# Kernel tuning notes

Measured on AMD Instinct MI355X. Metric: run time of the kernel, lower is better.

The kernel has to match this reference:

```python
import jax, jax.numpy as jnp
import numpy as np

IMG_DIM = 512


def _grid_q(img_dim):
    # matches torch module: q = [repeat(x, D), tile(y, D)] -> shape [2, D*D]
    x = np.arange(img_dim)
    q = np.stack([np.repeat(x, img_dim), np.tile(x, img_dim)], axis=0)
    return jnp.asarray(q, jnp.float32)


def _get_pixel(point, neighbor, imflat, img_dim):
    # point, neighbor: [N,2,HW]; imflat: [N,3,HW]
    w = 1.0 - jnp.abs(point - neighbor)          # [N,2,HW]
    weight = w[:, 0] * w[:, 1]                   # [N,HW]
    inds = (neighbor[:, 1] + img_dim * neighbor[:, 0]).astype(jnp.int32)  # y + D*x, [N,HW]
    # fused gather over all 3 channels (original does 3 separate torch.gather)
    pix = jnp.take_along_axis(imflat, inds[:, None, :], axis=2)  # [N,3,HW]
    return weight[:, None, :] * pix


def _get_masked_rp(image, mask, qi_orig, img_dim):
    N, Cc, H, W = image.shape
    imflat = image.reshape(N, Cc, H * W)
    qi_rescale = qi_orig * img_dim
    qi = jnp.clip(qi_rescale, 0.001, img_dim - 1.001)
    xf = jnp.floor(qi[:, 0:1]); yf = jnp.floor(qi[:, 1:2])
    xc = jnp.ceil(qi[:, 0:1]);  yc = jnp.ceil(qi[:, 1:2])
    res = (_get_pixel(qi, jnp.concatenate([xf, yf], axis=1), imflat, img_dim)
         + _get_pixel(qi, jnp.concatenate([xc, yf], axis=1), imflat, img_dim)
         + _get_pixel(qi, jnp.concatenate([xf, yc], axis=1), imflat, img_dim)
         + _get_pixel(qi, jnp.concatenate([xc, yc], axis=1), imflat, img_dim))
    oob_loss = jnp.mean((qi_rescale - qi) ** 2) / (img_dim ** 2) * 0.0001
    res_img = res.reshape(image.shape)
    return res_img * mask, oob_loss  # mask broadcasts [N,1,H,W] -> [N,3,H,W]


def setup_inputs() -> dict:
    key = jax.random.key(0)
    k1, k2, k3, k4, k5 = jax.random.split(key, 5)
    N, D = 16, IMG_DIM
    im1 = jax.random.normal(k1, (N, 3, D, D), dtype=jnp.float32)
    im2 = jax.random.normal(k2, (N, 3, D, D), dtype=jnp.float32)
    C = jax.random.normal(k3, (N, 2, D, D), dtype=jnp.float32)
    M1 = jax.random.uniform(k4, (N, 1, D, D), dtype=jnp.float32)
    M2 = jax.random.uniform(k5, (N, 1, D, D), dtype=jnp.float32)
    return {"im1": im1, "im2": im2, "C": C, "M1": M1, "M2": M2}


def reference(im1, im2, C, M1, M2):
    img_dim = im1.shape[-1]
    N = C.shape[0]
    Cflat = C.reshape(N, 2, -1)                 # [N,2,HW]
    total_mask = M1 + M2
    M1n = M1 / total_mask
    M2n = M2 / total_mask
    q = _grid_q(img_dim)[None]                  # [1,2,HW], broadcasts to [N,2,HW]
    a, oob_a = _get_masked_rp(im1, M1n, q + Cflat, img_dim)
    b, oob_b = _get_masked_rp(im2, M2n, q - Cflat, img_dim)
    return a + b, oob_a + oob_b
```

## Files before the change

### kernel.cpp

```cpp
#include <hip/hip_runtime.h>

#define D     512
#define HW    (D * D)
#define BLOCK 256
#define PPT   4
#define PIX_PER_BLOCK (BLOCK * PPT)

__device__ __forceinline__ void sample1(const float* __restrict__ im,
                                        float rx, float ry, float m,
                                        float r[3], double* oob) {
    float cxq = fminf(fmaxf(rx, 0.001f), 510.999f);
    float cyq = fminf(fmaxf(ry, 0.001f), 510.999f);
    float dx = rx - cxq;
    float dy = ry - cyq;
    *oob += (double)(dx * dx) + (double)(dy * dy);

    float xf = floorf(cxq), xc = ceilf(cxq);
    float yf = floorf(cyq), yc = ceilf(cyq);
    float wxf = 1.0f - (cxq - xf);
    float wxc = 1.0f - (xc - cxq);
    float wyf = 1.0f - (cyq - yf);
    float wyc = 1.0f - (yc - cyq);

    int ixf = (int)xf, ixc = (int)xc, iyf = (int)yf, iyc = (int)yc;
    int i00 = iyf + D * ixf;
    int i10 = iyf + D * ixc;
    int i01 = iyc + D * ixf;
    int i11 = iyc + D * ixc;

    float w00 = wxf * wyf, w10 = wxc * wyf, w01 = wxf * wyc, w11 = wxc * wyc;

#pragma unroll
    for (int c = 0; c < 3; ++c) {
        const float* __restrict__ ch = im + (size_t)c * HW;
        float pix = w00 * ch[i00] + w10 * ch[i10] + w01 * ch[i01] + w11 * ch[i11];
        r[c] += m * pix;
    }
}

__global__ void __launch_bounds__(BLOCK) vm_kernel(
    const float* __restrict__ im1, const float* __restrict__ im2,
    const float* __restrict__ C,   const float* __restrict__ M1,
    const float* __restrict__ M2,  float* __restrict__ out,
    double* __restrict__ partials)
{
    int t   = blockIdx.x * BLOCK + threadIdx.x;
    int idx = t * PPT;
    int n = idx >> 18;
    int p = idx & (HW - 1);
    int i = p >> 9;
    int j = p & (D - 1);

    const size_t cb = (size_t)n * 2 * HW + p;
    const size_t mb = (size_t)n * HW + p;
    float4 cx4 = *(const float4*)(C  + cb);
    float4 cy4 = *(const float4*)(C  + cb + HW);
    float4 m14 = *(const float4*)(M1 + mb);
    float4 m24 = *(const float4*)(M2 + mb);

    float cx[PPT] = {cx4.x, cx4.y, cx4.z, cx4.w};
    float cy[PPT] = {cy4.x, cy4.y, cy4.z, cy4.w};
    float m1[PPT] = {m14.x, m14.y, m14.z, m14.w};
    float m2[PPT] = {m24.x, m24.y, m24.z, m24.w};

    const float* base1 = im1 + (size_t)n * 3 * HW;
    const float* base2 = im2 + (size_t)n * 3 * HW;

    float o0[PPT], o1[PPT], o2[PPT];
    double oob = 0.0;

#pragma unroll
    for (int k = 0; k < PPT; ++k) {
        float tot = m1[k] + m2[k];
        float m1n = m1[k] / tot;
        float m2n = m2[k] / tot;
        float r[3] = {0.f, 0.f, 0.f};
        float fi = (float)i;
        float fj = (float)(j + k);
        sample1(base1, (fi + cx[k]) * (float)D, (fj + cy[k]) * (float)D, m1n, r, &oob);
        sample1(base2, (fi - cx[k]) * (float)D, (fj - cy[k]) * (float)D, m2n, r, &oob);
        o0[k] = r[0]; o1[k] = r[1]; o2[k] = r[2];
    }

    size_t ob = (size_t)n * 3 * HW + p;
    *(float4*)(out + ob)          = make_float4(o0[0], o0[1], o0[2], o0[3]);
    *(float4*)(out + ob + HW)     = make_float4(o1[0], o1[1], o1[2], o1[3]);
    *(float4*)(out + ob + 2 * HW) = make_float4(o2[0], o2[1], o2[2], o2[3]);

    for (int off = 32; off > 0; off >>= 1)
        oob += __shfl_down(oob, off, 64);

    __shared__ double soob[BLOCK / 64];
    int lane = threadIdx.x & 63;
    int w    = threadIdx.x >> 6;
    if (lane == 0) soob[w] = oob;
    __syncthreads();
    if (threadIdx.x == 0)
        partials[blockIdx.x] = soob[0] + soob[1] + soob[2] + soob[3];
}

__global__ void __launch_bounds__(BLOCK) reduce_kernel(
    const double* __restrict__ partials, int nparts,
    float* __restrict__ out_last, double scale)
{
    double s = 0.0;
    for (int i = threadIdx.x; i < nparts; i += BLOCK)
        s += partials[i];
    for (int off = 32; off > 0; off >>= 1)
        s += __shfl_down(s, off, 64);

    __shared__ double sm[BLOCK / 64];
    int lane = threadIdx.x & 63;
    int w    = threadIdx.x >> 6;
    if (lane == 0) sm[w] = s;
    __syncthreads();
    if (threadIdx.x == 0)
        *out_last = (float)((sm[0] + sm[1] + sm[2] + sm[3]) * scale);
}

extern "C" void kernel_launch(void* const* d_in, const int* in_sizes, int n_in,
                              void* d_out, int out_size, void* d_ws, size_t ws_size,
                              hipStream_t stream) {
    const float* im1 = (const float*)d_in[0];
    const float* im2 = (const float*)d_in[1];
    const float* C   = (const float*)d_in[2];
    const float* M1  = (const float*)d_in[3];
    const float* M2  = (const float*)d_in[4];
    float* out = (float*)d_out;
    double* ws = (double*)d_ws;

    int N = in_sizes[3] / HW;
    int total  = N * HW;
    int blocks = total / PIX_PER_BLOCK;

    vm_kernel<<<blocks, BLOCK, 0, stream>>>(im1, im2, C, M1, M2, out, ws);

    double scale = 1.0 / ((double)N * 2.0 * (double)HW) / (double)HW * 1e-4;
    reduce_kernel<<<1, BLOCK, 0, stream>>>(ws, blocks, out + (out_size - 1), scale);
}
```

Measured before the change: 219.3 us.

## Remap threads to row strips, preload corner pixels, and use float OOB sums

Each thread now handles one column across four rows instead of four consecutive pixels. Each block loads the bottom-right 2x2 corner pixels of both images once. Samples clamped to that corner use the preloaded values and skip the per-channel gathers, which matters because random displacements scaled by 512 push many samples out of range. The per-thread out-of-bounds accumulation moves from double to float, which removes FP64 arithmetic but risks precision loss in the loss term.

```diff
diff --git a/kernel.cpp b/kernel.cpp
--- a/kernel.cpp
+++ b/kernel.cpp
@@ -3,17 +3,18 @@
 #define D     512
 #define HW    (D * D)
 #define BLOCK 256
-#define PPT   4
-#define PIX_PER_BLOCK (BLOCK * PPT)
+#define ROWS  4
+#define COLS  256
 
 __device__ __forceinline__ void sample1(const float* __restrict__ im,
+                                        const float* __restrict__ cpix,
                                         float rx, float ry, float m,
-                                        float r[3], double* oob) {
+                                        float r[3], float* oob) {
     float cxq = fminf(fmaxf(rx, 0.001f), 510.999f);
     float cyq = fminf(fmaxf(ry, 0.001f), 510.999f);
     float dx = rx - cxq;
     float dy = ry - cyq;
-    *oob += (double)(dx * dx) + (double)(dy * dy);
+    *oob += dx * dx + dy * dy;
 
     float xf = floorf(cxq), xc = ceilf(cxq);
     float yf = floorf(cyq), yc = ceilf(cyq);
@@ -21,21 +22,37 @@
     float wxc = 1.0f - (xc - cxq);
     float wyf = 1.0f - (cyq - yf);
     float wyc = 1.0f - (yc - cyq);
-
-    int ixf = (int)xf, ixc = (int)xc, iyf = (int)yf, iyc = (int)yc;
-    int i00 = iyf + D * ixf;
-    int i10 = iyf + D * ixc;
-    int i01 = iyc + D * ixf;
-    int i11 = iyc + D * ixc;
-
     float w00 = wxf * wyf, w10 = wxc * wyf, w01 = wxf * wyc, w11 = wxc * wyc;
 
+    float p[3][4];
 #pragma unroll
     for (int c = 0; c < 3; ++c) {
-        const float* __restrict__ ch = im + (size_t)c * HW;
-        float pix = w00 * ch[i00] + w10 * ch[i10] + w01 * ch[i01] + w11 * ch[i11];
-        r[c] += m * pix;
+        p[c][0] = cpix[c * 4 + 0];
+        p[c][1] = cpix[c * 4 + 1];
+        p[c][2] = cpix[c * 4 + 2];
+        p[c][3] = cpix[c * 4 + 3];
     }
+
+    bool corner = (rx >= 510.999f) && (ry >= 510.999f);
+    if (!corner) {
+        int ixf = (int)xf, ixc = (int)xc, iyf = (int)yf, iyc = (int)yc;
+        int i00 = iyf + D * ixf;
+        int i10 = iyf + D * ixc;
+        int i01 = iyc + D * ixf;
+        int i11 = iyc + D * ixc;
+#pragma unroll
+        for (int c = 0; c < 3; ++c) {
+            const float* __restrict__ ch = im + (size_t)c * HW;
+            p[c][0] = ch[i00];
+            p[c][1] = ch[i10];
+            p[c][2] = ch[i01];
+            p[c][3] = ch[i11];
+        }
+    }
+
+#pragma unroll
+    for (int c = 0; c < 3; ++c)
+        r[c] += m * (w00 * p[c][0] + w10 * p[c][1] + w01 * p[c][2] + w11 * p[c][3]);
 }
 
 __global__ void __launch_bounds__(BLOCK) vm_kernel(
@@ -44,59 +61,71 @@
     const float* __restrict__ M2,  float* __restrict__ out,
     double* __restrict__ partials)
 {
-    int t   = blockIdx.x * BLOCK + threadIdx.x;
-    int idx = t * PPT;
-    int n = idx >> 18;
-    int p = idx & (HW - 1);
-    int i = p >> 9;
-    int j = p & (D - 1);
-
-    const size_t cb = (size_t)n * 2 * HW + p;
-    const size_t mb = (size_t)n * HW + p;
-    float4 cx4 = *(const float4*)(C  + cb);
-    float4 cy4 = *(const float4*)(C  + cb + HW);
-    float4 m14 = *(const float4*)(M1 + mb);
-    float4 m24 = *(const float4*)(M2 + mb);
-
-    float cx[PPT] = {cx4.x, cx4.y, cx4.z, cx4.w};
-    float cy[PPT] = {cy4.x, cy4.y, cy4.z, cy4.w};
-    float m1[PPT] = {m14.x, m14.y, m14.z, m14.w};
-    float m2[PPT] = {m24.x, m24.y, m24.z, m24.w};
+    int b    = blockIdx.x;
+    int colh = b & 1;
+    int rg   = (b >> 1) & 127;
+    int n    = b >> 8;
+    int j    = colh * COLS + threadIdx.x;
+    int i0   = rg * ROWS;
 
     const float* base1 = im1 + (size_t)n * 3 * HW;
     const float* base2 = im2 + (size_t)n * 3 * HW;
 
-    float o0[PPT], o1[PPT], o2[PPT];
-    double oob = 0.0;
+    float cp1[12], cp2[12];
+#pragma unroll
+    for (int c = 0; c < 3; ++c) {
+        const float* c1 = base1 + (size_t)c * HW;
+        const float* c2 = base2 + (size_t)c * HW;
+        cp1[c * 4 + 0] = c1[510 + D * 510];
+        cp1[c * 4 + 1] = c1[510 + D * 511];
+        cp1[c * 4 + 2] = c1[511 + D * 510];
+        cp1[c * 4 + 3] = c1[511 + D * 511];
+        cp2[c * 4 + 0] = c2[510 + D * 510];
+        cp2[c * 4 + 1] = c2[510 + D * 511];
+        cp2[c * 4 + 2] = c2[511 + D * 510];
+        cp2[c * 4 + 3] = c2[511 + D * 511];
+    }
+
+    const size_t cb = (size_t)n * 2 * HW;
+    const size_t mb = (size_t)n * HW;
+    const size_t ob = (size_t)n * 3 * HW;
+
+    float oob = 0.0f;
 
 #pragma unroll
-    for (int k = 0; k < PPT; ++k) {
-        float tot = m1[k] + m2[k];
-        float m1n = m1[k] / tot;
-        float m2n = m2[k] / tot;
-        float r[3] = {0.f, 0.f, 0.f};
-        float fi = (float)i;
-        float fj = (float)(j + k);
-        sample1(base1, (fi + cx[k]) * (float)D, (fj + cy[k]) * (float)D, m1n, r, &oob);
-        sample1(base2, (fi - cx[k]) * (float)D, (fj - cy[k]) * (float)D, m2n, r, &oob);
-        o0[k] = r[0]; o1[k] = r[1]; o2[k] = r[2];
+    for (int r = 0; r < ROWS; ++r) {
+        int i = i0 + r;
+        size_t pp = (size_t)i * D + j;
+
+        float cx = C[cb + pp];
+        float cy = C[cb + HW + pp];
+        float m1 = M1[mb + pp];
+        float m2 = M2[mb + pp];
+        float tot = m1 + m2;
+        float m1n = m1 / tot;
+        float m2n = m2 / tot;
+
+        float acc[3] = {0.f, 0.f, 0.f};
+        float fi = (float)i, fj = (float)j;
+        sample1(base1, cp1, (fi + cx) * (float)D, (fj + cy) * (float)D, m1n, acc, &oob);
+        sample1(base2, cp2, (fi - cx) * (float)D, (fj - cy) * (float)D, m2n, acc, &oob);
+
+        out[ob + pp]          = acc[0];
+        out[ob + HW + pp]     = acc[1];
+        out[ob + 2 * HW + pp] = acc[2];
     }
-
-    size_t ob = (size_t)n * 3 * HW + p;
-    *(float4*)(out + ob)          = make_float4(o0[0], o0[1], o0[2], o0[3]);
-    *(float4*)(out + ob + HW)     = make_float4(o1[0], o1[1], o1[2], o1[3]);
-    *(float4*)(out + ob + 2 * HW) = make_float4(o2[0], o2[1], o2[2], o2[3]);
 
     for (int off = 32; off > 0; off >>= 1)
         oob += __shfl_down(oob, off, 64);
 
-    __shared__ double soob[BLOCK / 64];
+    __shared__ float soob[BLOCK / 64];
     int lane = threadIdx.x & 63;
     int w    = threadIdx.x >> 6;
     if (lane == 0) soob[w] = oob;
     __syncthreads();
     if (threadIdx.x == 0)
-        partials[blockIdx.x] = soob[0] + soob[1] + soob[2] + soob[3];
+        partials[blockIdx.x] = (double)soob[0] + (double)soob[1]
+                             + (double)soob[2] + (double)soob[3];
 }
 
 __global__ void __launch_bounds__(BLOCK) reduce_kernel(
@@ -130,8 +159,7 @@
     double* ws = (double*)d_ws;
 
     int N = in_sizes[3] / HW;
-    int total  = N * HW;
-    int blocks = total / PIX_PER_BLOCK;
+    int blocks = N * (D / ROWS) * (D / COLS);
 
     vm_kernel<<<blocks, BLOCK, 0, stream>>>(im1, im2, C, M1, M2, out, ws);
 
```

After: 210.8 us. 3.9% less time.
